# Kernel optimization log

Hardware: AMD Instinct MI355X
Metric: run time of the kernel (lower is better)

The kernel has to match this reference:

```python
import jax, jax.numpy as jnp
import numpy as np

M_BLEND = 0.3
LR_REFINE = 0.1
N_REFINE = 10
N_SAMPLES = 256
USE_INFONCE = True
MARGIN = 0.2
TAU = 0.07


def safe_norm(x, eps=1e-8):
    return x / jnp.maximum(jnp.linalg.norm(x, axis=-1, keepdims=True), eps)


def setup_inputs() -> dict:
    key = jax.random.key(0)
    k1, k2, k3, k4 = jax.random.split(key, 4)
    fg_proto = safe_norm(jax.random.normal(k1, (64, 512), dtype=jnp.float32))
    bg_proto = safe_norm(jax.random.normal(k2, (64, 512), dtype=jnp.float32))
    F_map = jax.random.normal(k3, (16, 512, 96, 96), dtype=jnp.float32)
    M_map = jax.random.uniform(k4, (16, 96, 96), dtype=jnp.float32)
    return {"fg_proto": fg_proto, "bg_proto": bg_proto, "F_map": F_map, "M_map": M_map}


def _refine(feats, protos):
    # iterative k-means-like refinement: argmax assign -> per-cluster mean -> blended, renormalized centroid
    p = protos
    K = p.shape[0]
    ones = jnp.ones((feats.shape[0],), feats.dtype)
    for it in range(N_REFINE):
        step = LR_REFINE / (1.0 + 0.5 * it)
        assign = jnp.argmax(feats @ p.T, axis=1)                      # [S]
        sums = jax.ops.segment_sum(feats, assign, num_segments=K)    # [K, C]
        counts = jax.ops.segment_sum(ones, assign, num_segments=K)   # [K]
        cluster_mean = sums / jnp.maximum(counts, 1.0)[:, None]
        new_p = safe_norm((1.0 - step) * p + step * cluster_mean)
        p = jnp.where((counts > 0)[:, None], new_p, p)                # only update non-empty clusters
    return p


def reference(fg_proto, bg_proto, F_map, M_map):
    N, C, H, W = F_map.shape
    # M_map already at (H, W): nearest interpolation is identity; clamp to [0, 1]
    M_flat = jnp.clip(M_map.reshape(-1), 0.0, 1.0)                    # [N*H*W]
    F_flat = safe_norm(F_map.transpose(0, 2, 3, 1).reshape(-1, C))    # [N*H*W, C]

    sim_fg = F_flat @ fg_proto.T                                      # [P, Kf]
    sim_bg = F_flat @ bg_proto.T                                      # [P, Kb]
    dist_fg_min = 1.0 - sim_fg.max(axis=1)
    dist_bg_min = 1.0 - sim_bg.max(axis=1)

    k = min(N_SAMPLES, F_flat.shape[0])
    score_fg = jax.lax.stop_gradient(dist_fg_min * M_flat)
    score_bg = jax.lax.stop_gradient(dist_bg_min * (1.0 - M_flat))
    pos_idx = jax.lax.top_k(score_fg, k)[1]
    neg_idx = jax.lax.top_k(score_bg, k)[1]

    # refinement runs under no_grad in the original
    F_sg = jax.lax.stop_gradient(F_flat)
    p_fg = _refine(F_sg[pos_idx], jax.lax.stop_gradient(fg_proto))
    p_bg = _refine(F_sg[neg_idx], jax.lax.stop_gradient(bg_proto))

    # triplet loss (note: sim_neg also uses p_fg, as in the original)
    pos_feats = safe_norm(F_flat[pos_idx])
    neg_feats = safe_norm(F_flat[neg_idx])
    sim_pos = (pos_feats @ p_fg.T).max(axis=1).mean()
    sim_neg = (neg_feats @ p_fg.T).max(axis=1).mean()
    loss = jax.nn.relu(MARGIN + sim_neg - sim_pos)

    if USE_INFONCE:
        pos_sim = pos_feats @ p_fg.T / TAU                            # [k, Kf]
        neg_sim = pos_feats @ p_bg.T / TAU                            # [k, Kb]
        numerator = jax.scipy.special.logsumexp(pos_sim, axis=1)
        denominator = jax.scipy.special.logsumexp(jnp.concatenate([pos_sim, neg_sim], axis=1), axis=1)
        loss = loss + 0.25 * (-(numerator - denominator).mean())

    refined_fg = safe_norm((1.0 - M_BLEND) * fg_proto + M_BLEND * p_fg)
    refined_bg = safe_norm((1.0 - M_BLEND) * bg_proto + M_BLEND * p_bg)
    return loss, refined_fg, refined_bg
```

## Files before the change

kernel.cpp:

```cpp
#include <hip/hip_runtime.h>
#include <math.h>

#define P_TOTAL 147456
#define HW 9216
#define CHW (512*9216)
#define C_DIM 512
#define KP 64

__device__ __forceinline__ unsigned f2key(float f) {
    unsigned u = __float_as_uint(f);
    return (u & 0x80000000u) ? ~u : (u | 0x80000000u);
}

__global__ void k_init(const float* __restrict__ fg, const float* __restrict__ bg,
                       float* __restrict__ protoT, float* __restrict__ pwork) {
    int i = blockIdx.x * 256 + threadIdx.x;
    int side = i >> 15;
    int r = i & 32767;
    int k = r >> 9;
    int c = r & 511;
    float v = (side ? bg : fg)[k * 512 + c];
    protoT[side * 32768 + c * 64 + k] = v;
    pwork[side * 32768 + k * 512 + c] = v;
}

__global__ __launch_bounds__(256) void k_score(const float* __restrict__ F,
                                               const float* __restrict__ protoT,
                                               float* __restrict__ md_fg,
                                               float* __restrict__ md_bg,
                                               float* __restrict__ n2out) {
    __shared__ float lds[2048];
    const int side = blockIdx.y;
    const int p = blockIdx.x * 256 + threadIdx.x;
    const int n = p / HW;
    const int hw = p - n * HW;
    const float* Fp = F + (size_t)n * CHW + hw;
    const float* PT = protoT + side * (C_DIM * 64);

    float acc[64];
#pragma unroll
    for (int k = 0; k < 64; ++k) acc[k] = 0.f;
    float n2 = 0.f;

    for (int cc = 0; cc < 16; ++cc) {
        __syncthreads();
#pragma unroll
        for (int i = 0; i < 8; ++i)
            lds[threadIdx.x + 256 * i] = PT[cc * 2048 + threadIdx.x + 256 * i];
        __syncthreads();
        for (int c = 0; c < 32; ++c) {
            float f = Fp[(size_t)(cc * 32 + c) * HW];
            if (side == 0) n2 = fmaf(f, f, n2);
#pragma unroll
            for (int k = 0; k < 64; ++k) acc[k] = fmaf(f, lds[c * 64 + k], acc[k]);
        }
    }
    float m = acc[0];
#pragma unroll
    for (int k = 1; k < 64; ++k) m = fmaxf(m, acc[k]);
    if (side == 0) { md_fg[p] = m; n2out[p] = n2; }
    else          { md_bg[p] = m; }
}

__global__ void k_combine(const float* __restrict__ M,
                          float* __restrict__ sfg, float* __restrict__ sbg,
                          float* __restrict__ n2inv) {
    int p = blockIdx.x * 256 + threadIdx.x;
    float inv = 1.f / fmaxf(sqrtf(n2inv[p]), 1e-8f);
    float m = fminf(fmaxf(M[p], 0.f), 1.f);
    float sf = (1.f - sfg[p] * inv) * m;
    float sb = (1.f - sbg[p] * inv) * (1.f - m);
    sfg[p] = sf; sbg[p] = sb; n2inv[p] = inv;
}

__global__ void k_hist1(const float* __restrict__ sfg, const float* __restrict__ sbg,
                        unsigned* __restrict__ hist) {
    int side = blockIdx.y;
    int p = blockIdx.x * 256 + threadIdx.x;
    float s = side ? sbg[p] : sfg[p];
    atomicAdd(&hist[side * 65536 + (f2key(s) >> 16)], 1u);
}

__global__ void k_hist2(const float* __restrict__ sfg, const float* __restrict__ sbg,
                        const int* __restrict__ ctrl, unsigned* __restrict__ hist2) {
    int side = blockIdx.y;
    int p = blockIdx.x * 256 + threadIdx.x;
    float s = side ? sbg[p] : sfg[p];
    unsigned key = f2key(s);
    if ((int)(key >> 16) == ctrl[side * 8 + 0])
        atomicAdd(&hist2[side * 65536 + (key & 0xffffu)], 1u);
}

__global__ __launch_bounds__(1024) void k_scan(const unsigned* __restrict__ hist,
                                               int* __restrict__ ctrl, int pass) {
    __shared__ unsigned sd[1024];
    int side = blockIdx.x;
    const unsigned* h = hist + side * 65536;
    int t = threadIdx.x;
    unsigned partial = 0;
    for (int j = 0; j < 64; ++j) partial += h[65535 - (t * 64 + j)];
    sd[t] = partial;
    __syncthreads();
    for (int off = 1; off < 1024; off <<= 1) {
        unsigned v = (t >= off) ? sd[t - off] : 0u;
        __syncthreads();
        sd[t] += v;
        __syncthreads();
    }
    unsigned incl = sd[t];
    unsigned excl = incl - partial;
    unsigned target = (pass == 0) ? 256u : (unsigned)ctrl[side * 8 + 1];
    if (excl < target && target <= incl) {
        unsigned cum = excl;
        for (int j = 0; j < 64; ++j) {
            int b = 65535 - (t * 64 + j);
            unsigned c = h[b];
            if (cum + c >= target) {
                if (pass == 0) {
                    ctrl[side * 8 + 0] = b;
                    ctrl[side * 8 + 1] = (int)(target - cum);
                } else {
                    unsigned vkey = ((unsigned)ctrl[side * 8 + 0] << 16) | (unsigned)b;
                    ctrl[side * 8 + 2] = (int)vkey;
                    int n_gt = (int)(256u - (unsigned)ctrl[side * 8 + 1] + cum);
                    ctrl[side * 8 + 3] = n_gt;
                    ctrl[side * 8 + 4] = 256 - n_gt;
                }
                break;
            }
            cum += c;
        }
    }
}

__global__ void k_collect(const float* __restrict__ sfg, const float* __restrict__ sbg,
                          int* __restrict__ ctrl, int* __restrict__ idx, int* __restrict__ ties) {
    int side = blockIdx.y;
    int p = blockIdx.x * 256 + threadIdx.x;
    float s = side ? sbg[p] : sfg[p];
    unsigned key = f2key(s);
    unsigned vkey = (unsigned)ctrl[side * 8 + 2];
    if (key > vkey) {
        int pos = atomicAdd(&ctrl[side * 8 + 5], 1);
        idx[side * 256 + pos] = p;
    } else if (key == vkey) {
        int pos = atomicAdd(&ctrl[side * 8 + 6], 1);
        if (pos < 512) ties[side * 512 + pos] = p;
    }
}

__global__ void k_finalize(int* __restrict__ ctrl, int* __restrict__ idx, int* __restrict__ ties) {
    int side = threadIdx.x;
    if (side >= 2) return;
    int n_gt = ctrl[side * 8 + 3];
    int need = ctrl[side * 8 + 4];
    int cnt = ctrl[side * 8 + 6];
    if (cnt > 512) cnt = 512;
    int* tb = ties + side * 512;
    for (int q = 0; q < need; ++q) {
        int mi = q;
        for (int j = q + 1; j < cnt; ++j) if (tb[j] < tb[mi]) mi = j;
        int tmp = tb[q]; tb[q] = tb[mi]; tb[mi] = tmp;
        idx[side * 256 + n_gt + q] = tb[q];
    }
}

__global__ void k_gather(const float* __restrict__ F, const float* __restrict__ inv,
                         const int* __restrict__ idx, float* __restrict__ feats) {
    int b = blockIdx.x;
    int side = b >> 8, j = b & 255;
    int p = idx[side * 256 + j];
    float iv = inv[p];
    int n = p / HW, hw = p - n * HW;
    const float* Fp = F + (size_t)n * CHW + hw;
    float* o = feats + (size_t)(side * 256 + j) * 512;
    for (int c = threadIdx.x; c < 512; c += 256)
        o[c] = Fp[(size_t)c * HW] * iv;
}

__global__ __launch_bounds__(256) void k_assign(const float* __restrict__ feats,
                                                const float* __restrict__ pwork,
                                                float* __restrict__ sums,
                                                float* __restrict__ counts) {
    int w = blockIdx.x * 4 + (threadIdx.x >> 6);
    int lane = threadIdx.x & 63;
    int side = w >> 8, j = w & 255;
    const float4* fr = (const float4*)(feats + (size_t)(side * 256 + j) * 512);
    const float4* pw = (const float4*)(pwork + (size_t)side * 32768 + (size_t)lane * 512);
    float dot = 0.f;
#pragma unroll 4
    for (int c = 0; c < 128; ++c) {
        float4 a = fr[c], b = pw[c];
        dot = fmaf(a.x, b.x, dot); dot = fmaf(a.y, b.y, dot);
        dot = fmaf(a.z, b.z, dot); dot = fmaf(a.w, b.w, dot);
    }
    float bv = dot; int bi = lane;
#pragma unroll
    for (int m = 32; m >= 1; m >>= 1) {
        float ov = __shfl_xor(bv, m);
        int oi = __shfl_xor(bi, m);
        if (ov > bv || (ov == bv && oi < bi)) { bv = ov; bi = oi; }
    }
    if (lane == 0) atomicAdd(&counts[side * 64 + bi], 1.f);
    const float* frf = feats + (size_t)(side * 256 + j) * 512;
    float* srow = sums + (size_t)side * 32768 + (size_t)bi * 512;
#pragma unroll
    for (int i = 0; i < 8; ++i) {
        int c = lane + i * 64;
        atomicAdd(&srow[c], frf[c]);
    }
}

__global__ __launch_bounds__(64) void k_update(float* __restrict__ pwork,
                                               float* __restrict__ sums,
                                               float* __restrict__ counts,
                                               float step) {
    int side = blockIdx.x >> 6, k = blockIdx.x & 63;
    int lane = threadIdx.x;
    float cnt = counts[side * 64 + k];
    float* srow = sums + (size_t)side * 32768 + (size_t)k * 512;
    float* prow = pwork + (size_t)side * 32768 + (size_t)k * 512;
    float bl[8]; float n2 = 0.f;
#pragma unroll
    for (int i = 0; i < 8; ++i) {
        int c = lane + i * 64;
        float mean = srow[c] / fmaxf(cnt, 1.f);
        float v = (1.f - step) * prow[c] + step * mean;
        bl[i] = v; n2 = fmaf(v, v, n2);
        srow[c] = 0.f;
    }
#pragma unroll
    for (int m = 32; m >= 1; m >>= 1) n2 += __shfl_xor(n2, m);
    float inv = 1.f / fmaxf(sqrtf(n2), 1e-8f);
    if (cnt > 0.f) {
#pragma unroll
        for (int i = 0; i < 8; ++i) prow[lane + i * 64] = bl[i] * inv;
    }
    if (lane == 0) counts[side * 64 + k] = 0.f;
}

__global__ __launch_bounds__(256) void k_losspart(const float* __restrict__ feats,
                                                  const float* __restrict__ pwork,
                                                  float* __restrict__ lpart) {
    int w = blockIdx.x * 4 + (threadIdx.x >> 6);
    int lane = threadIdx.x & 63;
    int half = w >> 8, j = w & 255;
    const float4* fr = (const float4*)(feats + (size_t)(half * 256 + j) * 512);
    const float4* pf = (const float4*)(pwork + (size_t)lane * 512);
    const float4* pb = (const float4*)(pwork + 32768 + (size_t)lane * 512);
    if (half == 0) {
        float d1 = 0.f, d2 = 0.f;
        for (int c = 0; c < 128; ++c) {
            float4 a = fr[c], x = pf[c], y = pb[c];
            d1 = fmaf(a.x, x.x, d1); d1 = fmaf(a.y, x.y, d1);
            d1 = fmaf(a.z, x.z, d1); d1 = fmaf(a.w, x.w, d1);
            d2 = fmaf(a.x, y.x, d2); d2 = fmaf(a.y, y.y, d2);
            d2 = fmaf(a.z, y.z, d2); d2 = fmaf(a.w, y.w, d2);
        }
        float smax = d1;
        for (int m = 32; m >= 1; m >>= 1) smax = fmaxf(smax, __shfl_xor(smax, m));
        float a = d1 / 0.07f, b = d2 / 0.07f;
        float m1 = a;
        for (int m = 32; m >= 1; m >>= 1) m1 = fmaxf(m1, __shfl_xor(m1, m));
        float mb = b;
        for (int m = 32; m >= 1; m >>= 1) mb = fmaxf(mb, __shfl_xor(mb, m));
        float md = fmaxf(m1, mb);
        float sn = expf(a - m1);
        for (int m = 32; m >= 1; m >>= 1) sn += __shfl_xor(sn, m);
        float sdn = expf(a - md) + expf(b - md);
        for (int m = 32; m >= 1; m >>= 1) sdn += __shfl_xor(sdn, m);
        float num = m1 + logf(sn);
        float den = md + logf(sdn);
        if (lane == 0) { lpart[j] = smax; lpart[512 + j] = num - den; }
    } else {
        float d1 = 0.f;
        for (int c = 0; c < 128; ++c) {
            float4 a = fr[c], x = pf[c];
            d1 = fmaf(a.x, x.x, d1); d1 = fmaf(a.y, x.y, d1);
            d1 = fmaf(a.z, x.z, d1); d1 = fmaf(a.w, x.w, d1);
        }
        float smax = d1;
        for (int m = 32; m >= 1; m >>= 1) smax = fmaxf(smax, __shfl_xor(smax, m));
        if (lane == 0) lpart[256 + j] = smax;
    }
}

__global__ __launch_bounds__(256) void k_final(const float* __restrict__ lpart,
                                               float* __restrict__ out) {
    __shared__ float red[3][4];
    int t = threadIdx.x;
    float sp = lpart[t], sn = lpart[256 + t], nm = lpart[512 + t];
    for (int m = 32; m >= 1; m >>= 1) {
        sp += __shfl_xor(sp, m); sn += __shfl_xor(sn, m); nm += __shfl_xor(nm, m);
    }
    int wv = t >> 6;
    if ((t & 63) == 0) { red[0][wv] = sp; red[1][wv] = sn; red[2][wv] = nm; }
    __syncthreads();
    if (t == 0) {
        float SP = 0, SN = 0, NM = 0;
        for (int i = 0; i < 4; ++i) { SP += red[0][i]; SN += red[1][i]; NM += red[2][i]; }
        SP /= 256.f; SN /= 256.f; NM /= 256.f;
        out[0] = fmaxf(0.f, 0.2f + SN - SP) + 0.25f * (-NM);
    }
}

__global__ __launch_bounds__(64) void k_refined(const float* __restrict__ fg,
                                                const float* __restrict__ bg,
                                                const float* __restrict__ pwork,
                                                float* __restrict__ out) {
    int side = blockIdx.x >> 6, k = blockIdx.x & 63;
    int lane = threadIdx.x;
    const float* proto = (side ? bg : fg) + (size_t)k * 512;
    const float* prow = pwork + (size_t)side * 32768 + (size_t)k * 512;
    float bl[8]; float n2 = 0.f;
#pragma unroll
    for (int i = 0; i < 8; ++i) {
        int c = lane + i * 64;
        float v = 0.7f * proto[c] + 0.3f * prow[c];
        bl[i] = v; n2 = fmaf(v, v, n2);
    }
#pragma unroll
    for (int m = 32; m >= 1; m >>= 1) n2 += __shfl_xor(n2, m);
    float inv = 1.f / fmaxf(sqrtf(n2), 1e-8f);
    float* o = out + 1 + (size_t)side * 32768 + (size_t)k * 512;
#pragma unroll
    for (int i = 0; i < 8; ++i) o[lane + i * 64] = bl[i] * inv;
}

extern "C" void kernel_launch(void* const* d_in, const int* in_sizes, int n_in,
                              void* d_out, int out_size, void* d_ws, size_t ws_size,
                              hipStream_t stream) {
    const float* fg = (const float*)d_in[0];
    const float* bg = (const float*)d_in[1];
    const float* F  = (const float*)d_in[2];
    const float* M  = (const float*)d_in[3];
    float* out = (float*)d_out;
    char* ws = (char*)d_ws;

    size_t o = 0;
    auto alloc = [&](size_t bytes) { size_t r = o; o += (bytes + 1023) & ~(size_t)1023; return r; };
    size_t off_hist1 = alloc(2 * 65536 * 4);
    size_t off_hist2 = alloc(2 * 65536 * 4);
    size_t off_ctrl  = alloc(64);
    size_t off_cnts  = alloc(2 * 64 * 4);
    size_t off_sums  = alloc(2 * 64 * 512 * 4);
    size_t zbytes = o;
    size_t off_sfg   = alloc(P_TOTAL * 4);
    size_t off_sbg   = alloc(P_TOTAL * 4);
    size_t off_n2    = alloc(P_TOTAL * 4);
    size_t off_pT    = alloc(2 * 512 * 64 * 4);
    size_t off_idx   = alloc(2 * 256 * 4);
    size_t off_ties  = alloc(2 * 512 * 4);
    size_t off_feats = alloc(2 * 256 * 512 * 4);
    size_t off_pwork = alloc(2 * 64 * 512 * 4);
    size_t off_lpart = alloc(768 * 4);

    unsigned* hist1 = (unsigned*)(ws + off_hist1);
    unsigned* hist2 = (unsigned*)(ws + off_hist2);
    int* ctrl   = (int*)(ws + off_ctrl);
    float* cnts = (float*)(ws + off_cnts);
    float* sums = (float*)(ws + off_sums);
    float* sfg  = (float*)(ws + off_sfg);
    float* sbg  = (float*)(ws + off_sbg);
    float* n2   = (float*)(ws + off_n2);
    float* pT   = (float*)(ws + off_pT);
    int* idx    = (int*)(ws + off_idx);
    int* ties   = (int*)(ws + off_ties);
    float* feats = (float*)(ws + off_feats);
    float* pwork = (float*)(ws + off_pwork);
    float* lpart = (float*)(ws + off_lpart);

    hipMemsetAsync(ws, 0, zbytes, stream);
    k_init<<<256, 256, 0, stream>>>(fg, bg, pT, pwork);
    k_score<<<dim3(576, 2), 256, 0, stream>>>(F, pT, sfg, sbg, n2);
    k_combine<<<576, 256, 0, stream>>>(M, sfg, sbg, n2);
    k_hist1<<<dim3(576, 2), 256, 0, stream>>>(sfg, sbg, hist1);
    k_scan<<<2, 1024, 0, stream>>>(hist1, ctrl, 0);
    k_hist2<<<dim3(576, 2), 256, 0, stream>>>(sfg, sbg, ctrl, hist2);
    k_scan<<<2, 1024, 0, stream>>>(hist2, ctrl, 1);
    k_collect<<<dim3(576, 2), 256, 0, stream>>>(sfg, sbg, ctrl, idx, ties);
    k_finalize<<<1, 64, 0, stream>>>(ctrl, idx, ties);
    k_gather<<<512, 256, 0, stream>>>(F, n2, idx, feats);
    for (int it = 0; it < 10; ++it) {
        k_assign<<<128, 256, 0, stream>>>(feats, pwork, sums, cnts);
        k_update<<<128, 64, 0, stream>>>(pwork, sums, cnts, (float)(0.1 / (1.0 + 0.5 * it)));
    }
    k_losspart<<<128, 256, 0, stream>>>(feats, pwork, lpart);
    k_final<<<1, 256, 0, stream>>>(lpart, out);
    k_refined<<<128, 64, 0, stream>>>(fg, bg, pwork, out);
}
```

Baseline: 1.139 ms.

## Fuse score, combine and histogram; merge refinement loop into one persistent kernel

The score kernel now handles both prototype sets in one pass. Each block covers 576 pixels with register tiling (9 pixels x 16 prototypes per thread) and software-prefetched channel loads. It also folds in the norm, mask combine and first histogram pass, so the feature map is read once instead of twice and three small kernels disappear. The 10-iteration refinement, loss and refined-prototype output become one 128-block kernel synchronised by a hand-rolled grid barrier on an atomic counter, removing about 23 launches. The barrier relies on all 128 blocks being resident at once and uses relaxed atomics with fences, which risks deadlock or ordering bugs.

Result: slower. 1.299 ms (+14.1%).

```diff
diff --git a/kernel.cpp b/kernel.cpp
--- a/kernel.cpp
+++ b/kernel.cpp
@@ -4,91 +4,135 @@
 #define P_TOTAL 147456
 #define HW 9216
 #define CHW (512*9216)
-#define C_DIM 512
-#define KP 64
+#define NBR 128
 
 __device__ __forceinline__ unsigned f2key(float f) {
     unsigned u = __float_as_uint(f);
     return (u & 0x80000000u) ? ~u : (u | 0x80000000u);
 }
 
+__device__ __forceinline__ float agload(const float* p) {
+    return __hip_atomic_load(p, __ATOMIC_RELAXED, __HIP_MEMORY_SCOPE_AGENT);
+}
+__device__ __forceinline__ void agstoref(float* p, float v) {
+    __hip_atomic_store(p, v, __ATOMIC_RELAXED, __HIP_MEMORY_SCOPE_AGENT);
+}
+
 __global__ void k_init(const float* __restrict__ fg, const float* __restrict__ bg,
-                       float* __restrict__ protoT, float* __restrict__ pwork) {
+                       float* __restrict__ protoT, float* __restrict__ pworkT) {
     int i = blockIdx.x * 256 + threadIdx.x;
     int side = i >> 15;
     int r = i & 32767;
     int k = r >> 9;
     int c = r & 511;
     float v = (side ? bg : fg)[k * 512 + c];
-    protoT[side * 32768 + c * 64 + k] = v;
-    pwork[side * 32768 + k * 512 + c] = v;
-}
-
-__global__ __launch_bounds__(256) void k_score(const float* __restrict__ F,
-                                               const float* __restrict__ protoT,
-                                               float* __restrict__ md_fg,
-                                               float* __restrict__ md_bg,
-                                               float* __restrict__ n2out) {
-    __shared__ float lds[2048];
-    const int side = blockIdx.y;
-    const int p = blockIdx.x * 256 + threadIdx.x;
-    const int n = p / HW;
-    const int hw = p - n * HW;
-    const float* Fp = F + (size_t)n * CHW + hw;
-    const float* PT = protoT + side * (C_DIM * 64);
-
-    float acc[64];
-#pragma unroll
-    for (int k = 0; k < 64; ++k) acc[k] = 0.f;
-    float n2 = 0.f;
-
-    for (int cc = 0; cc < 16; ++cc) {
-        __syncthreads();
-#pragma unroll
-        for (int i = 0; i < 8; ++i)
-            lds[threadIdx.x + 256 * i] = PT[cc * 2048 + threadIdx.x + 256 * i];
-        __syncthreads();
-        for (int c = 0; c < 32; ++c) {
-            float f = Fp[(size_t)(cc * 32 + c) * HW];
-            if (side == 0) n2 = fmaf(f, f, n2);
-#pragma unroll
-            for (int k = 0; k < 64; ++k) acc[k] = fmaf(f, lds[c * 64 + k], acc[k]);
-        }
-    }
-    float m = acc[0];
-#pragma unroll
-    for (int k = 1; k < 64; ++k) m = fmaxf(m, acc[k]);
-    if (side == 0) { md_fg[p] = m; n2out[p] = n2; }
-    else          { md_bg[p] = m; }
-}
-
-__global__ void k_combine(const float* __restrict__ M,
-                          float* __restrict__ sfg, float* __restrict__ sbg,
-                          float* __restrict__ n2inv) {
-    int p = blockIdx.x * 256 + threadIdx.x;
-    float inv = 1.f / fmaxf(sqrtf(n2inv[p]), 1e-8f);
-    float m = fminf(fmaxf(M[p], 0.f), 1.f);
-    float sf = (1.f - sfg[p] * inv) * m;
-    float sb = (1.f - sbg[p] * inv) * (1.f - m);
-    sfg[p] = sf; sbg[p] = sb; n2inv[p] = inv;
-}
-
-__global__ void k_hist1(const float* __restrict__ sfg, const float* __restrict__ sbg,
-                        unsigned* __restrict__ hist) {
-    int side = blockIdx.y;
-    int p = blockIdx.x * 256 + threadIdx.x;
-    float s = side ? sbg[p] : sfg[p];
-    atomicAdd(&hist[side * 65536 + (f2key(s) >> 16)], 1u);
-}
-
-__global__ void k_hist2(const float* __restrict__ sfg, const float* __restrict__ sbg,
-                        const int* __restrict__ ctrl, unsigned* __restrict__ hist2) {
-    int side = blockIdx.y;
-    int p = blockIdx.x * 256 + threadIdx.x;
-    float s = side ? sbg[p] : sfg[p];
-    unsigned key = f2key(s);
-    if ((int)(key >> 16) == ctrl[side * 8 + 0])
-        atomicAdd(&hist2[side * 65536 + (key & 0xffffu)], 1u);
+    protoT[c * 128 + side * 64 + k] = v;
+    pworkT[side * 32768 + c * 64 + k] = v;
+}
+
+__global__ __launch_bounds__(512, 2) void k_score(const float* __restrict__ F,
+                                                  const float* __restrict__ protoT,
+                                                  const float* __restrict__ M,
+                                                  float* __restrict__ sfg,
+                                                  float* __restrict__ sbg,
+                                                  float* __restrict__ invout,
+                                                  unsigned* __restrict__ hist) {
+    __shared__ float lds[8192];
+    const int t = threadIdx.x;
+    const int lane = t & 63;
+    const int w = t >> 6;
+    const int p0 = blockIdx.x * 576 + lane;
+    const int n = p0 / HW;
+    const int hw0 = p0 - n * HW;
+    const float* Fb = F + (size_t)n * CHW;
+
+    float acc[16][9];
+#pragma unroll
+    for (int jj = 0; jj < 16; ++jj)
+#pragma unroll
+        for (int i = 0; i < 9; ++i) acc[jj][i] = 0.f;
+    float nn[9];
+#pragma unroll
+    for (int i = 0; i < 9; ++i) nn[i] = 0.f;
+
+    auto ldch = [&](float (&dst)[9], int ch) {
+        int chc = ch > 511 ? 511 : ch;
+        const float* q = Fb + hw0 + (size_t)chc * HW;
+#pragma unroll
+        for (int i = 0; i < 9; ++i) dst[i] = q[i * 64];
+    };
+    auto kstep = [&](const float (&f)[9], int cc) {
+        const float4* pv4 = (const float4*)(lds + cc * 128 + w * 16);
+#pragma unroll
+        for (int j4 = 0; j4 < 4; ++j4) {
+            float4 bq = pv4[j4];
+#pragma unroll
+            for (int i = 0; i < 9; ++i) {
+                acc[j4 * 4 + 0][i] = fmaf(f[i], bq.x, acc[j4 * 4 + 0][i]);
+                acc[j4 * 4 + 1][i] = fmaf(f[i], bq.y, acc[j4 * 4 + 1][i]);
+                acc[j4 * 4 + 2][i] = fmaf(f[i], bq.z, acc[j4 * 4 + 2][i]);
+                acc[j4 * 4 + 3][i] = fmaf(f[i], bq.w, acc[j4 * 4 + 3][i]);
+            }
+        }
+    };
+
+    float fa[9], fb[9];
+    ldch(fa, 0); ldch(fb, 1);
+    int ch = 2;
+
+    for (int chunk = 0; chunk < 8; ++chunk) {
+        __syncthreads();
+        {
+            const float4* src = (const float4*)(protoT + chunk * 8192);
+            float4* dst = (float4*)lds;
+#pragma unroll
+            for (int i2 = 0; i2 < 4; ++i2) dst[t + 512 * i2] = src[t + 512 * i2];
+        }
+        __syncthreads();
+        for (int c2 = 0; c2 < 32; ++c2) {
+            if (w == 0) {
+#pragma unroll
+                for (int i = 0; i < 9; ++i) nn[i] = fmaf(fa[i], fa[i], nn[i]);
+            }
+            kstep(fa, c2 * 2);
+            ldch(fa, ch++);
+            if (w == 0) {
+#pragma unroll
+                for (int i = 0; i < 9; ++i) nn[i] = fmaf(fb[i], fb[i], nn[i]);
+            }
+            kstep(fb, c2 * 2 + 1);
+            ldch(fb, ch++);
+        }
+    }
+
+    float m16[9];
+#pragma unroll
+    for (int i = 0; i < 9; ++i) {
+        float mm = acc[0][i];
+#pragma unroll
+        for (int jj = 1; jj < 16; ++jj) mm = fmaxf(mm, acc[jj][i]);
+        m16[i] = mm;
+    }
+    __syncthreads();
+#pragma unroll
+    for (int i = 0; i < 9; ++i) lds[w * 576 + i * 64 + lane] = m16[i];
+    if (w == 0) {
+#pragma unroll
+        for (int i = 0; i < 9; ++i) lds[4608 + i * 64 + lane] = nn[i];
+    }
+    __syncthreads();
+    for (int pi = t; pi < 576; pi += 512) {
+        int p = blockIdx.x * 576 + pi;
+        float fgm = fmaxf(fmaxf(lds[pi], lds[576 + pi]), fmaxf(lds[1152 + pi], lds[1728 + pi]));
+        float bgm = fmaxf(fmaxf(lds[2304 + pi], lds[2880 + pi]), fmaxf(lds[3456 + pi], lds[4032 + pi]));
+        float inv = 1.f / fmaxf(sqrtf(lds[4608 + pi]), 1e-8f);
+        float mm = fminf(fmaxf(M[p], 0.f), 1.f);
+        float sf = (1.f - fgm * inv) * mm;
+        float sb = (1.f - bgm * inv) * (1.f - mm);
+        sfg[p] = sf; sbg[p] = sb; invout[p] = inv;
+        atomicAdd(&hist[f2key(sf) >> 16], 1u);
+        atomicAdd(&hist[65536 + (f2key(sb) >> 16)], 1u);
+    }
 }
 
 __global__ __launch_bounds__(1024) void k_scan(const unsigned* __restrict__ hist,
@@ -133,6 +177,16 @@
     }
 }
 
+__global__ void k_hist2(const float* __restrict__ sfg, const float* __restrict__ sbg,
+                        const int* __restrict__ ctrl, unsigned* __restrict__ hist2) {
+    int side = blockIdx.y;
+    int p = blockIdx.x * 256 + threadIdx.x;
+    float s = side ? sbg[p] : sfg[p];
+    unsigned key = f2key(s);
+    if ((int)(key >> 16) == ctrl[side * 8 + 0])
+        atomicAdd(&hist2[side * 65536 + (key & 0xffffu)], 1u);
+}
+
 __global__ void k_collect(const float* __restrict__ sfg, const float* __restrict__ sbg,
                           int* __restrict__ ctrl, int* __restrict__ idx, int* __restrict__ ties) {
     int side = blockIdx.y;
@@ -178,85 +232,157 @@
         o[c] = Fp[(size_t)c * HW] * iv;
 }
 
-__global__ __launch_bounds__(256) void k_assign(const float* __restrict__ feats,
-                                                const float* __restrict__ pwork,
+__global__ __launch_bounds__(256) void k_refine(const float* __restrict__ feats,
+                                                float* __restrict__ pworkT,
                                                 float* __restrict__ sums,
-                                                float* __restrict__ counts) {
-    int w = blockIdx.x * 4 + (threadIdx.x >> 6);
-    int lane = threadIdx.x & 63;
-    int side = w >> 8, j = w & 255;
-    const float4* fr = (const float4*)(feats + (size_t)(side * 256 + j) * 512);
-    const float4* pw = (const float4*)(pwork + (size_t)side * 32768 + (size_t)lane * 512);
-    float dot = 0.f;
-#pragma unroll 4
-    for (int c = 0; c < 128; ++c) {
-        float4 a = fr[c], b = pw[c];
-        dot = fmaf(a.x, b.x, dot); dot = fmaf(a.y, b.y, dot);
-        dot = fmaf(a.z, b.z, dot); dot = fmaf(a.w, b.w, dot);
-    }
-    float bv = dot; int bi = lane;
-#pragma unroll
-    for (int m = 32; m >= 1; m >>= 1) {
-        float ov = __shfl_xor(bv, m);
-        int oi = __shfl_xor(bi, m);
-        if (ov > bv || (ov == bv && oi < bi)) { bv = ov; bi = oi; }
-    }
-    if (lane == 0) atomicAdd(&counts[side * 64 + bi], 1.f);
-    const float* frf = feats + (size_t)(side * 256 + j) * 512;
-    float* srow = sums + (size_t)side * 32768 + (size_t)bi * 512;
-#pragma unroll
-    for (int i = 0; i < 8; ++i) {
-        int c = lane + i * 64;
-        atomicAdd(&srow[c], frf[c]);
-    }
-}
-
-__global__ __launch_bounds__(64) void k_update(float* __restrict__ pwork,
-                                               float* __restrict__ sums,
-                                               float* __restrict__ counts,
-                                               float step) {
-    int side = blockIdx.x >> 6, k = blockIdx.x & 63;
-    int lane = threadIdx.x;
-    float cnt = counts[side * 64 + k];
-    float* srow = sums + (size_t)side * 32768 + (size_t)k * 512;
-    float* prow = pwork + (size_t)side * 32768 + (size_t)k * 512;
-    float bl[8]; float n2 = 0.f;
-#pragma unroll
-    for (int i = 0; i < 8; ++i) {
-        int c = lane + i * 64;
-        float mean = srow[c] / fmaxf(cnt, 1.f);
-        float v = (1.f - step) * prow[c] + step * mean;
-        bl[i] = v; n2 = fmaf(v, v, n2);
-        srow[c] = 0.f;
-    }
-#pragma unroll
-    for (int m = 32; m >= 1; m >>= 1) n2 += __shfl_xor(n2, m);
-    float inv = 1.f / fmaxf(sqrtf(n2), 1e-8f);
-    if (cnt > 0.f) {
-#pragma unroll
-        for (int i = 0; i < 8; ++i) prow[lane + i * 64] = bl[i] * inv;
-    }
-    if (lane == 0) counts[side * 64 + k] = 0.f;
-}
-
-__global__ __launch_bounds__(256) void k_losspart(const float* __restrict__ feats,
-                                                  const float* __restrict__ pwork,
-                                                  float* __restrict__ lpart) {
-    int w = blockIdx.x * 4 + (threadIdx.x >> 6);
-    int lane = threadIdx.x & 63;
-    int half = w >> 8, j = w & 255;
-    const float4* fr = (const float4*)(feats + (size_t)(half * 256 + j) * 512);
-    const float4* pf = (const float4*)(pwork + (size_t)lane * 512);
-    const float4* pb = (const float4*)(pwork + 32768 + (size_t)lane * 512);
-    if (half == 0) {
-        float d1 = 0.f, d2 = 0.f;
-        for (int c = 0; c < 128; ++c) {
-            float4 a = fr[c], x = pf[c], y = pb[c];
-            d1 = fmaf(a.x, x.x, d1); d1 = fmaf(a.y, x.y, d1);
-            d1 = fmaf(a.z, x.z, d1); d1 = fmaf(a.w, x.w, d1);
-            d2 = fmaf(a.x, y.x, d2); d2 = fmaf(a.y, y.y, d2);
-            d2 = fmaf(a.z, y.z, d2); d2 = fmaf(a.w, y.w, d2);
-        }
+                                                float* __restrict__ counts,
+                                                const float* __restrict__ fg,
+                                                const float* __restrict__ bg,
+                                                float* __restrict__ lpart,
+                                                float* __restrict__ out,
+                                                int* __restrict__ bar) {
+    __shared__ float lds[16384];
+    const int t = threadIdx.x;
+    const int lane = t & 63;
+    const int w = t >> 6;
+    const int blk = blockIdx.x;
+    const int side = blk >> 6;
+    const int kk = blk & 63;
+    const int row = blk * 4 + w;
+    const int j = row & 255;
+    const float4* fr4 = (const float4*)(feats + (size_t)row * 512);
+    const float* frf = feats + (size_t)row * 512;
+
+    auto gbar = [&](int e) {
+        __syncthreads();
+        __threadfence();
+        if (t == 0) {
+            atomicAdd(bar, 1);
+            while (__hip_atomic_load(bar, __ATOMIC_RELAXED, __HIP_MEMORY_SCOPE_AGENT) < e * NBR)
+                __builtin_amdgcn_s_sleep(2);
+        }
+        __syncthreads();
+        __threadfence();
+    };
+    auto stage = [&](int s, int h) {
+        const float* src = pworkT + (size_t)s * 32768 + (size_t)h * 16384;
+        float4* d = (float4*)lds;
+#pragma unroll
+        for (int q = 0; q < 16; ++q) {
+            int e4 = t + 256 * q;
+            const float* s4 = src + (size_t)e4 * 4;
+            float x0 = agload(s4), x1 = agload(s4 + 1), x2 = agload(s4 + 2), x3 = agload(s4 + 3);
+            d[e4] = make_float4(x0, x1, x2, x3);
+        }
+    };
+    auto dot_half = [&](int h) -> float {
+        float d = 0.f;
+#pragma unroll 8
+        for (int c4 = 0; c4 < 64; ++c4) {
+            float4 a = fr4[h * 64 + c4];
+            int base = c4 * 256 + lane;
+            d = fmaf(a.x, lds[base], d);
+            d = fmaf(a.y, lds[base + 64], d);
+            d = fmaf(a.z, lds[base + 128], d);
+            d = fmaf(a.w, lds[base + 192], d);
+        }
+        return d;
+    };
+
+    int ep = 0;
+    for (int it = 0; it < 10; ++it) {
+        stage(side, 0);
+        __syncthreads();
+        float dot = dot_half(0);
+        __syncthreads();
+        stage(side, 1);
+        __syncthreads();
+        dot += dot_half(1);
+
+        float bv = dot; int bi = lane;
+#pragma unroll
+        for (int m = 32; m >= 1; m >>= 1) {
+            float ov = __shfl_xor(bv, m);
+            int oi = __shfl_xor(bi, m);
+            if (ov > bv || (ov == bv && oi < bi)) { bv = ov; bi = oi; }
+        }
+        if (lane == 0) atomicAdd(&counts[side * 64 + bi], 1.f);
+        float* srow = sums + (size_t)side * 32768 + (size_t)bi * 512;
+#pragma unroll
+        for (int i = 0; i < 8; ++i) {
+            int c = lane + i * 64;
+            atomicAdd(&srow[c], frf[c]);
+        }
+        gbar(++ep);
+
+        if (t < 64) {
+            float cnt = agload(&counts[side * 64 + kk]);
+            float* srow2 = sums + (size_t)side * 32768 + (size_t)kk * 512;
+            float* pw = pworkT + (size_t)side * 32768;
+            float step = (float)(0.1 / (1.0 + 0.5 * (double)it));
+            float bl[8]; float n2 = 0.f;
+#pragma unroll
+            for (int i = 0; i < 8; ++i) {
+                int c = t + i * 64;
+                float s = agload(&srow2[c]);
+                float mean = s / fmaxf(cnt, 1.f);
+                float pv = agload(&pw[(size_t)c * 64 + kk]);
+                float v = (1.f - step) * pv + step * mean;
+                bl[i] = v; n2 = fmaf(v, v, n2);
+                agstoref(&srow2[c], 0.f);
+            }
+#pragma unroll
+            for (int m = 32; m >= 1; m >>= 1) n2 += __shfl_xor(n2, m);
+            float inv = 1.f / fmaxf(sqrtf(n2), 1e-8f);
+            if (cnt > 0.f) {
+#pragma unroll
+                for (int i = 0; i < 8; ++i) {
+                    int c = t + i * 64;
+                    agstoref(&pw[(size_t)c * 64 + kk], bl[i] * inv);
+                }
+            }
+            if (t == 0) agstoref(&counts[side * 64 + kk], 0.f);
+        }
+        gbar(++ep);
+    }
+
+    if (t < 64) {
+        const float* proto = (side ? bg : fg) + (size_t)kk * 512;
+        const float* pw = pworkT + (size_t)side * 32768;
+        float bl[8]; float n2 = 0.f;
+#pragma unroll
+        for (int i = 0; i < 8; ++i) {
+            int c = t + i * 64;
+            float v = 0.7f * proto[c] + 0.3f * agload(&pw[(size_t)c * 64 + kk]);
+            bl[i] = v; n2 = fmaf(v, v, n2);
+        }
+#pragma unroll
+        for (int m = 32; m >= 1; m >>= 1) n2 += __shfl_xor(n2, m);
+        float inv = 1.f / fmaxf(sqrtf(n2), 1e-8f);
+#pragma unroll
+        for (int i = 0; i < 8; ++i)
+            out[1 + side * 32768 + kk * 512 + t + i * 64] = bl[i] * inv;
+    }
+
+    stage(0, 0);
+    __syncthreads();
+    float d1 = dot_half(0);
+    __syncthreads();
+    stage(0, 1);
+    __syncthreads();
+    d1 += dot_half(1);
+    float d2 = 0.f;
+    if (side == 0) {
+        __syncthreads();
+        stage(1, 0);
+        __syncthreads();
+        d2 = dot_half(0);
+        __syncthreads();
+        stage(1, 1);
+        __syncthreads();
+        d2 += dot_half(1);
+    }
+    if (side == 0) {
         float smax = d1;
         for (int m = 32; m >= 1; m >>= 1) smax = fmaxf(smax, __shfl_xor(smax, m));
         float a = d1 / 0.07f, b = d2 / 0.07f;
@@ -271,60 +397,29 @@
         for (int m = 32; m >= 1; m >>= 1) sdn += __shfl_xor(sdn, m);
         float num = m1 + logf(sn);
         float den = md + logf(sdn);
-        if (lane == 0) { lpart[j] = smax; lpart[512 + j] = num - den; }
+        if (lane == 0) { agstoref(&lpart[j], smax); agstoref(&lpart[512 + j], num - den); }
     } else {
-        float d1 = 0.f;
-        for (int c = 0; c < 128; ++c) {
-            float4 a = fr[c], x = pf[c];
-            d1 = fmaf(a.x, x.x, d1); d1 = fmaf(a.y, x.y, d1);
-            d1 = fmaf(a.z, x.z, d1); d1 = fmaf(a.w, x.w, d1);
-        }
         float smax = d1;
         for (int m = 32; m >= 1; m >>= 1) smax = fmaxf(smax, __shfl_xor(smax, m));
-        if (lane == 0) lpart[256 + j] = smax;
-    }
-}
-
-__global__ __launch_bounds__(256) void k_final(const float* __restrict__ lpart,
-                                               float* __restrict__ out) {
-    __shared__ float red[3][4];
-    int t = threadIdx.x;
-    float sp = lpart[t], sn = lpart[256 + t], nm = lpart[512 + t];
-    for (int m = 32; m >= 1; m >>= 1) {
-        sp += __shfl_xor(sp, m); sn += __shfl_xor(sn, m); nm += __shfl_xor(nm, m);
-    }
-    int wv = t >> 6;
-    if ((t & 63) == 0) { red[0][wv] = sp; red[1][wv] = sn; red[2][wv] = nm; }
-    __syncthreads();
-    if (t == 0) {
-        float SP = 0, SN = 0, NM = 0;
-        for (int i = 0; i < 4; ++i) { SP += red[0][i]; SN += red[1][i]; NM += red[2][i]; }
-        SP /= 256.f; SN /= 256.f; NM /= 256.f;
-        out[0] = fmaxf(0.f, 0.2f + SN - SP) + 0.25f * (-NM);
-    }
-}
-
-__global__ __launch_bounds__(64) void k_refined(const float* __restrict__ fg,
-                                                const float* __restrict__ bg,
-                                                const float* __restrict__ pwork,
-                                                float* __restrict__ out) {
-    int side = blockIdx.x >> 6, k = blockIdx.x & 63;
-    int lane = threadIdx.x;
-    const float* proto = (side ? bg : fg) + (size_t)k * 512;
-    const float* prow = pwork + (size_t)side * 32768 + (size_t)k * 512;
-    float bl[8]; float n2 = 0.f;
-#pragma unroll
-    for (int i = 0; i < 8; ++i) {
-        int c = lane + i * 64;
-        float v = 0.7f * proto[c] + 0.3f * prow[c];
-        bl[i] = v; n2 = fmaf(v, v, n2);
-    }
-#pragma unroll
-    for (int m = 32; m >= 1; m >>= 1) n2 += __shfl_xor(n2, m);
-    float inv = 1.f / fmaxf(sqrtf(n2), 1e-8f);
-    float* o = out + 1 + (size_t)side * 32768 + (size_t)k * 512;
-#pragma unroll
-    for (int i = 0; i < 8; ++i) o[lane + i * 64] = bl[i] * inv;
+        if (lane == 0) agstoref(&lpart[256 + j], smax);
+    }
+    gbar(++ep);
+
+    if (blk == 0) {
+        float sp = agload(&lpart[t]), sn = agload(&lpart[256 + t]), nm = agload(&lpart[512 + t]);
+#pragma unroll
+        for (int m = 32; m >= 1; m >>= 1) {
+            sp += __shfl_xor(sp, m); sn += __shfl_xor(sn, m); nm += __shfl_xor(nm, m);
+        }
+        if ((t & 63) == 0) { lds[w] = sp; lds[8 + w] = sn; lds[16 + w] = nm; }
+        __syncthreads();
+        if (t == 0) {
+            float SP = 0, SN = 0, NM = 0;
+            for (int i = 0; i < 4; ++i) { SP += lds[i]; SN += lds[8 + i]; NM += lds[16 + i]; }
+            SP /= 256.f; SN /= 256.f; NM /= 256.f;
+            out[0] = fmaxf(0.f, 0.2f + SN - SP) + 0.25f * (-NM);
+        }
+    }
 }
 
 extern "C" void kernel_launch(void* const* d_in, const int* in_sizes, int n_in,
@@ -344,11 +439,12 @@
     size_t off_ctrl  = alloc(64);
     size_t off_cnts  = alloc(2 * 64 * 4);
     size_t off_sums  = alloc(2 * 64 * 512 * 4);
+    size_t off_bar   = alloc(64);
     size_t zbytes = o;
     size_t off_sfg   = alloc(P_TOTAL * 4);
     size_t off_sbg   = alloc(P_TOTAL * 4);
-    size_t off_n2    = alloc(P_TOTAL * 4);
-    size_t off_pT    = alloc(2 * 512 * 64 * 4);
+    size_t off_inv   = alloc(P_TOTAL * 4);
+    size_t off_pT    = alloc(512 * 128 * 4);
     size_t off_idx   = alloc(2 * 256 * 4);
     size_t off_ties  = alloc(2 * 512 * 4);
     size_t off_feats = alloc(2 * 256 * 512 * 4);
@@ -360,32 +456,25 @@
     int* ctrl   = (int*)(ws + off_ctrl);
     float* cnts = (float*)(ws + off_cnts);
     float* sums = (float*)(ws + off_sums);
+    int* bar    = (int*)(ws + off_bar);
     float* sfg  = (float*)(ws + off_sfg);
     float* sbg  = (float*)(ws + off_sbg);
-    float* n2   = (float*)(ws + off_n2);
+    float* inv  = (float*)(ws + off_inv);
     float* pT   = (float*)(ws + off_pT);
     int* idx    = (int*)(ws + off_idx);
     int* ties   = (int*)(ws + off_ties);
     float* feats = (float*)(ws + off_feats);
-    float* pwork = (float*)(ws + off_pwork);
+    float* pworkT = (float*)(ws + off_pwork);
     float* lpart = (float*)(ws + off_lpart);
 
     hipMemsetAsync(ws, 0, zbytes, stream);
-    k_init<<<256, 256, 0, stream>>>(fg, bg, pT, pwork);
-    k_score<<<dim3(576, 2), 256, 0, stream>>>(F, pT, sfg, sbg, n2);
-    k_combine<<<576, 256, 0, stream>>>(M, sfg, sbg, n2);
-    k_hist1<<<dim3(576, 2), 256, 0, stream>>>(sfg, sbg, hist1);
+    k_init<<<256, 256, 0, stream>>>(fg, bg, pT, pworkT);
+    k_score<<<256, 512, 0, stream>>>(F, pT, M, sfg, sbg, inv, hist1);
     k_scan<<<2, 1024, 0, stream>>>(hist1, ctrl, 0);
     k_hist2<<<dim3(576, 2), 256, 0, stream>>>(sfg, sbg, ctrl, hist2);
     k_scan<<<2, 1024, 0, stream>>>(hist2, ctrl, 1);
     k_collect<<<dim3(576, 2), 256, 0, stream>>>(sfg, sbg, ctrl, idx, ties);
     k_finalize<<<1, 64, 0, stream>>>(ctrl, idx, ties);
-    k_gather<<<512, 256, 0, stream>>>(F, n2, idx, feats);
-    for (int it = 0; it < 10; ++it) {
-        k_assign<<<128, 256, 0, stream>>>(feats, pwork, sums, cnts);
-        k_update<<<128, 64, 0, stream>>>(pwork, sums, cnts, (float)(0.1 / (1.0 + 0.5 * it)));
-    }
-    k_losspart<<<128, 256, 0, stream>>>(feats, pwork, lpart);
-    k_final<<<1, 256, 0, stream>>>(lpart, out);
-    k_refined<<<128, 64, 0, stream>>>(fg, bg, pwork, out);
-}
+    k_gather<<<512, 256, 0, stream>>>(F, inv, idx, feats);
+    k_refine<<<128, 256, 0, stream>>>(feats, pworkT, sums, cnts, fg, bg, lpart, out, bar);
+}
```
